# Kernel optimization log

Measured on AMD Instinct MI355X. Metric: run time of the kernel, lower is better.

The kernel has to match this reference:

```python
import jax, jax.numpy as jnp
import numpy as np

N_NODES = 10000
AVG_DEG = 32
N_FEAT = 512
HIDDEN = 32
CODE = 16


def setup_inputs() -> dict:
    key = jax.random.key(0)
    k1, k2, k3, k4, k5 = jax.random.split(key, 5)
    E = N_NODES * AVG_DEG
    src = jax.random.randint(k1, (E,), 0, N_NODES, dtype=jnp.int32)
    dst = jax.random.randint(k2, (E,), 0, N_NODES, dtype=jnp.int32)
    # A + I: add self loops (Kipf & Welling transform)
    loop = jnp.arange(N_NODES, dtype=jnp.int32)
    src = jnp.concatenate([src, loop])
    dst = jnp.concatenate([dst, loop])
    ones = jnp.ones(src.shape[0], jnp.float32)
    deg_row = jax.ops.segment_sum(ones, dst, num_segments=N_NODES)
    deg_col = jax.ops.segment_sum(ones, src, num_segments=N_NODES)
    # symmetric normalization D^-1/2 (A+I) D^-1/2
    edge_weight = jax.lax.rsqrt(deg_row[dst] * deg_col[src])
    x = jax.random.normal(k3, (N_NODES, N_FEAT), dtype=jnp.float32)
    W1 = jax.random.normal(k4, (N_FEAT, HIDDEN), dtype=jnp.float32) * 0.1
    W2 = jax.random.normal(k5, (HIDDEN, CODE), dtype=jnp.float32) * 0.1
    return {"x": x, "W1": W1, "W2": W2, "edge_weight": edge_weight,
            "src": src, "dst": dst}


def _spmm(edge_weight, src, dst, X):
    # sparse A_hat @ X via gather + weighted scatter-add
    return jax.ops.segment_sum(edge_weight[:, None] * X[src], dst,
                               num_segments=X.shape[0])


def reference(x, W1, W2, edge_weight, src, dst):
    # layer 1: A_hat @ (x @ W1), relu  (dropout inactive: eval mode)
    h = jax.nn.relu(_spmm(edge_weight, src, dst, x @ W1))
    # layer 2 (encoder): A_hat @ (h @ W2)
    z = _spmm(edge_weight, src, dst, h @ W2)  # [N, code]
    # inner-product decoder: sigmoid(Z Z^T)
    return jax.nn.sigmoid(jnp.einsum('nc,mc->nm', z, z))
```

## Files before the change

kernel.cpp:

```cpp
#include <hip/hip_runtime.h>
#include <hip/hip_bf16.h>

#define N_NODES 10000
#define N_FEAT  512
#define HIDDEN  32
#define CODE    16

typedef __attribute__((ext_vector_type(8))) short  short8;
typedef __attribute__((ext_vector_type(4))) float  floatx4;

__device__ __forceinline__ float bf2f(unsigned short h) {
    return __uint_as_float(((unsigned int)h) << 16);
}
__device__ __forceinline__ unsigned short f2bf(float f) {
    unsigned int u = __float_as_uint(f);
    u += 0x7fffu + ((u >> 16) & 1u);
    return (unsigned short)(u >> 16);
}
__device__ __forceinline__ float load_f(const void* p, size_t i, int isf32) {
    return isf32 ? ((const float*)p)[i] : bf2f(((const unsigned short*)p)[i]);
}
__device__ __forceinline__ int get_idx(const int* p, int e, int is64) {
    return is64 ? p[2 * (size_t)e] : p[e];
}

__global__ __launch_bounds__(384) void k_detect(const unsigned short* __restrict__ t0,
                                                const unsigned short* __restrict__ t1,
                                                const unsigned short* __restrict__ t2,
                                                const unsigned short* __restrict__ t3,
                                                const int* __restrict__ i0,
                                                const int* __restrict__ i1,
                                                int* __restrict__ flags) {
    const int w    = threadIdx.x >> 6;
    const int lane = threadIdx.x & 63;
    unsigned int m = 0;
    if (w < 4) {
        const unsigned short* p = (w == 0) ? t0 : (w == 1) ? t1 : (w == 2) ? t2 : t3;
        for (int i = lane; i < 128; i += 64) {
            unsigned int v = (unsigned int)p[2 * i] & 0x7fffu;
            m = m > v ? m : v;
        }
    } else {
        const int* p = (w == 4) ? i0 : i1;
        for (int i = lane; i < 128; i += 64) {
            m |= (unsigned int)p[2 * i + 1];
        }
    }
#pragma unroll
    for (int off = 32; off > 0; off >>= 1) {
        unsigned int o = (unsigned int)__shfl_down((int)m, off, 64);
        m = (w < 4) ? (m > o ? m : o) : (m | o);
    }
    if (lane == 0) flags[w] = (w < 4) ? (m >= 0x5000u ? 1 : 0) : (m == 0u ? 1 : 0);
}

__global__ __launch_bounds__(256) void k_xw1(const void* __restrict__ x,
                                             const void* __restrict__ W1,
                                             float* __restrict__ XW1,
                                             const int* __restrict__ flags) {
    const int xf32  = flags[0];
    const int w1f32 = flags[1];
    int t = blockIdx.x * 256 + threadIdx.x;
    if (t >= N_NODES * HIDDEN) return;
    const int n = t >> 5;
    const int c = t & 31;
    float acc = 0.f;
#pragma unroll 8
    for (int k = 0; k < N_FEAT; ++k) {
        float a = load_f(x,  (size_t)n * N_FEAT + k, xf32);
        float b = load_f(W1, (size_t)k * HIDDEN + c, w1f32);
        acc += a * b;
    }
    XW1[t] = acc;
}

__global__ __launch_bounds__(256) void k_spmm32(const void* __restrict__ ew,
                                                const int* __restrict__ src,
                                                const int* __restrict__ dst,
                                                const float* __restrict__ Xin,
                                                float* __restrict__ Hacc, int E,
                                                const int* __restrict__ flags) {
    const int ewf32 = flags[3];
    const int s64   = flags[4];
    const int d64   = flags[5];
    int t = blockIdx.x * 256 + threadIdx.x;
    int e = t >> 5;
    int f = t & 31;
    if (e >= E) return;
    float w = load_f(ew, e, ewf32);
    int   s = get_idx(src, e, s64);
    int   d = get_idx(dst, e, d64);
    float v = Xin[(size_t)s * HIDDEN + f] * w;
    atomicAdd(&Hacc[(size_t)d * HIDDEN + f], v);
}

__global__ __launch_bounds__(256) void k_hw2(const float* __restrict__ H,
                                             const void* __restrict__ W2,
                                             float* __restrict__ HW2,
                                             const int* __restrict__ flags) {
    const int w2f32 = flags[2];
    int t = blockIdx.x * 256 + threadIdx.x;
    if (t >= N_NODES * CODE) return;
    int n = t >> 4;
    int c = t & 15;
    float acc = 0.f;
#pragma unroll
    for (int k = 0; k < HIDDEN; ++k) {
        float h = H[n * HIDDEN + k];
        h = h > 0.f ? h : 0.f;
        acc += h * load_f(W2, k * CODE + c, w2f32);
    }
    HW2[t] = acc;
}

__global__ __launch_bounds__(256) void k_spmm16(const void* __restrict__ ew,
                                                const int* __restrict__ src,
                                                const int* __restrict__ dst,
                                                const float* __restrict__ Hin,
                                                float* __restrict__ Zacc, int E,
                                                const int* __restrict__ flags) {
    const int ewf32 = flags[3];
    const int s64   = flags[4];
    const int d64   = flags[5];
    int t = blockIdx.x * 256 + threadIdx.x;
    int e = t >> 4;
    int f = t & 15;
    if (e >= E) return;
    float w = load_f(ew, e, ewf32);
    int   s = get_idx(src, e, s64);
    int   d = get_idx(dst, e, d64);
    float v = Hin[(size_t)s * CODE + f] * w;
    atomicAdd(&Zacc[(size_t)d * CODE + f], v);
}

__global__ __launch_bounds__(256) void k_cvt(const float* __restrict__ Z,
                                             unsigned short* __restrict__ zb) {
    int t = blockIdx.x * 256 + threadIdx.x;
    if (t >= N_NODES * CODE) return;
    zb[t] = f2bf(Z[t]);
}

__global__ __launch_bounds__(256) void k_dec(const unsigned short* __restrict__ zb,
                                             float* __restrict__ out) {
    const int wave = threadIdx.x >> 6;
    const int lane = threadIdx.x & 63;
    const int l16  = lane & 15;
    const int quad = lane >> 4;

    const int r0 = blockIdx.y * 64 + wave * 16;
    const int c0 = blockIdx.x * 64;

    const short8 zero8 = {0, 0, 0, 0, 0, 0, 0, 0};

    int ra = r0 + l16;
    if (ra > N_NODES - 1) ra = N_NODES - 1;
    short8 afr = zero8;
    if (quad < 2) afr = *(const short8*)(zb + (size_t)ra * CODE + quad * 8);

    floatx4 acc[4];
#pragma unroll
    for (int t = 0; t < 4; ++t) {
        int cb = c0 + t * 16 + l16;
        if (cb > N_NODES - 1) cb = N_NODES - 1;
        short8 bfr = zero8;
        if (quad < 2) bfr = *(const short8*)(zb + (size_t)cb * CODE + quad * 8);
        floatx4 z4 = {0.f, 0.f, 0.f, 0.f};
        acc[t] = __builtin_amdgcn_mfma_f32_16x16x32_bf16(afr, bfr, z4, 0, 0, 0);
    }

#pragma unroll
    for (int t = 0; t < 4; ++t) {
        int col = c0 + t * 16 + l16;
#pragma unroll
        for (int r = 0; r < 4; ++r) {
            int row = r0 + quad * 4 + r;
            float s  = acc[t][r];
            float e  = __builtin_amdgcn_exp2f(-1.442695041f * s);
            float sg = __builtin_amdgcn_rcpf(1.f + e);
            if (row < N_NODES && col < N_NODES) {
                out[(size_t)row * N_NODES + col] = sg;
            }
        }
    }
}

extern "C" void kernel_launch(void* const* d_in, const int* in_sizes, int n_in,
                              void* d_out, int out_size, void* d_ws, size_t ws_size,
                              hipStream_t stream) {
    const void* x  = d_in[0];
    const void* W1 = d_in[1];
    const void* W2 = d_in[2];
    const void* ew = d_in[3];
    const int* src = (const int*)d_in[4];
    const int* dst = (const int*)d_in[5];
    float* out = (float*)d_out;
    const int E = in_sizes[3];

    float* ws   = (float*)d_ws;
    float* XW1  = ws;
    float* Hacc = ws + 320000;
    float* HW2  = ws;
    float* Zacc = ws + 160000;
    unsigned short* zb = (unsigned short*)(ws + 320000);
    int* flags = (int*)(ws + 640000);

    hipMemsetAsync(Hacc, 0, 320000 * sizeof(float), stream);

    k_detect<<<1, 384, 0, stream>>>((const unsigned short*)x,
                                    (const unsigned short*)W1,
                                    (const unsigned short*)W2,
                                    (const unsigned short*)ew,
                                    src, dst, flags);

    k_xw1<<<(N_NODES * HIDDEN + 255) / 256, 256, 0, stream>>>(x, W1, XW1, flags);
    k_spmm32<<<(E * 32 + 255) / 256, 256, 0, stream>>>(ew, src, dst, XW1, Hacc, E, flags);
    hipMemsetAsync(Zacc, 0, 160000 * sizeof(float), stream);
    k_hw2<<<(N_NODES * CODE + 255) / 256, 256, 0, stream>>>(Hacc, W2, HW2, flags);
    k_spmm16<<<(E * 16 + 255) / 256, 256, 0, stream>>>(ew, src, dst, HW2, Zacc, E, flags);
    k_cvt<<<(N_NODES * CODE + 255) / 256, 256, 0, stream>>>(Zacc, zb);

    dim3 grid((N_NODES + 63) / 64, (N_NODES + 63) / 64);
    k_dec<<<grid, 256, 0, stream>>>(zb, out);
}
```

Measured before the change: 569.2 us.

## Replace atomic scatter SpMM with per-call CSR build and row gather

Builds a CSR view of the edges on every call: a histogram of destinations, a single-block scan, and an atomic scatter of source indices and weights. Both SpMM layers then become row-wise gathers with no float atomics. The ReLU is folded into the first gather and the bf16 conversion into the second, which drops a kernel and two memsets. The decoder relies on Z Z^T being symmetric and writes the transposed tile as 4-wide vector stores. The trade-off is three extra small kernels (one of them a serial single-block scan) and a non-deterministic edge order within each row.

```diff
diff --git a/kernel.cpp b/kernel.cpp
--- a/kernel.cpp
+++ b/kernel.cpp
@@ -54,6 +54,60 @@
     if (lane == 0) flags[w] = (w < 4) ? (m >= 0x5000u ? 1 : 0) : (m == 0u ? 1 : 0);
 }
 
+__global__ __launch_bounds__(256) void k_hist(const int* __restrict__ dst,
+                                              int* __restrict__ cnt, int E,
+                                              const int* __restrict__ flags) {
+    const int d64 = flags[5];
+    int t = blockIdx.x * 256 + threadIdx.x;
+    if (t >= E) return;
+    atomicAdd(&cnt[get_idx(dst, t, d64)], 1);
+}
+
+__global__ __launch_bounds__(256) void k_scan(const int* __restrict__ cnt,
+                                              int* __restrict__ rowptr) {
+    __shared__ int sdata[256];
+    const int t = threadIdx.x;
+    const int base = t * 40;
+    int p = 0;
+    for (int j = 0; j < 40; ++j) {
+        int i = base + j;
+        if (i < N_NODES) p += cnt[i];
+    }
+    sdata[t] = p;
+    __syncthreads();
+    for (int off = 1; off < 256; off <<= 1) {
+        int v = (t >= off) ? sdata[t - off] : 0;
+        __syncthreads();
+        sdata[t] += v;
+        __syncthreads();
+    }
+    int run = sdata[t] - p;
+    for (int j = 0; j < 40; ++j) {
+        int i = base + j;
+        if (i < N_NODES) { rowptr[i] = run; run += cnt[i]; }
+    }
+    if (t == 255) rowptr[N_NODES] = sdata[255];
+}
+
+__global__ __launch_bounds__(256) void k_scatter(const int* __restrict__ src,
+                                                 const int* __restrict__ dst,
+                                                 const void* __restrict__ ew,
+                                                 const int* __restrict__ rowptr,
+                                                 int* __restrict__ fill,
+                                                 int* __restrict__ srcS,
+                                                 float* __restrict__ wS, int E,
+                                                 const int* __restrict__ flags) {
+    const int ewf32 = flags[3];
+    const int s64   = flags[4];
+    const int d64   = flags[5];
+    int t = blockIdx.x * 256 + threadIdx.x;
+    if (t >= E) return;
+    int d = get_idx(dst, t, d64);
+    int pos = rowptr[d] + atomicAdd(&fill[d], 1);
+    srcS[pos] = get_idx(src, t, s64);
+    wS[pos]   = load_f(ew, t, ewf32);
+}
+
 __global__ __launch_bounds__(256) void k_xw1(const void* __restrict__ x,
                                              const void* __restrict__ W1,
                                              float* __restrict__ XW1,
@@ -74,24 +128,22 @@
     XW1[t] = acc;
 }
 
-__global__ __launch_bounds__(256) void k_spmm32(const void* __restrict__ ew,
-                                                const int* __restrict__ src,
-                                                const int* __restrict__ dst,
-                                                const float* __restrict__ Xin,
-                                                float* __restrict__ Hacc, int E,
-                                                const int* __restrict__ flags) {
-    const int ewf32 = flags[3];
-    const int s64   = flags[4];
-    const int d64   = flags[5];
-    int t = blockIdx.x * 256 + threadIdx.x;
-    int e = t >> 5;
-    int f = t & 31;
-    if (e >= E) return;
-    float w = load_f(ew, e, ewf32);
-    int   s = get_idx(src, e, s64);
-    int   d = get_idx(dst, e, d64);
-    float v = Xin[(size_t)s * HIDDEN + f] * w;
-    atomicAdd(&Hacc[(size_t)d * HIDDEN + f], v);
+__global__ __launch_bounds__(256) void k_gather32(const int* __restrict__ rowptr,
+                                                  const int* __restrict__ srcS,
+                                                  const float* __restrict__ wS,
+                                                  const float* __restrict__ XW1,
+                                                  float* __restrict__ Hacc) {
+    const int lane = threadIdx.x & 63;
+    const int gw   = blockIdx.x * 4 + (threadIdx.x >> 6);
+    const int n    = gw * 2 + (lane >> 5);
+    const int f    = lane & 31;
+    if (n >= N_NODES) return;
+    const int s0 = rowptr[n], s1 = rowptr[n + 1];
+    float acc = 0.f;
+    for (int j = s0; j < s1; ++j) {
+        acc += wS[j] * XW1[(size_t)srcS[j] * HIDDEN + f];
+    }
+    Hacc[(size_t)n * HIDDEN + f] = fmaxf(acc, 0.f);
 }
 
 __global__ __launch_bounds__(256) void k_hw2(const float* __restrict__ H,
@@ -106,38 +158,27 @@
     float acc = 0.f;
 #pragma unroll
     for (int k = 0; k < HIDDEN; ++k) {
-        float h = H[n * HIDDEN + k];
-        h = h > 0.f ? h : 0.f;
-        acc += h * load_f(W2, k * CODE + c, w2f32);
+        acc += H[n * HIDDEN + k] * load_f(W2, k * CODE + c, w2f32);
     }
     HW2[t] = acc;
 }
 
-__global__ __launch_bounds__(256) void k_spmm16(const void* __restrict__ ew,
-                                                const int* __restrict__ src,
-                                                const int* __restrict__ dst,
-                                                const float* __restrict__ Hin,
-                                                float* __restrict__ Zacc, int E,
-                                                const int* __restrict__ flags) {
-    const int ewf32 = flags[3];
-    const int s64   = flags[4];
-    const int d64   = flags[5];
-    int t = blockIdx.x * 256 + threadIdx.x;
-    int e = t >> 4;
-    int f = t & 15;
-    if (e >= E) return;
-    float w = load_f(ew, e, ewf32);
-    int   s = get_idx(src, e, s64);
-    int   d = get_idx(dst, e, d64);
-    float v = Hin[(size_t)s * CODE + f] * w;
-    atomicAdd(&Zacc[(size_t)d * CODE + f], v);
-}
-
-__global__ __launch_bounds__(256) void k_cvt(const float* __restrict__ Z,
-                                             unsigned short* __restrict__ zb) {
-    int t = blockIdx.x * 256 + threadIdx.x;
-    if (t >= N_NODES * CODE) return;
-    zb[t] = f2bf(Z[t]);
+__global__ __launch_bounds__(256) void k_gather16(const int* __restrict__ rowptr,
+                                                  const int* __restrict__ srcS,
+                                                  const float* __restrict__ wS,
+                                                  const float* __restrict__ HW2,
+                                                  unsigned short* __restrict__ zb) {
+    const int lane = threadIdx.x & 63;
+    const int gw   = blockIdx.x * 4 + (threadIdx.x >> 6);
+    const int n    = gw * 4 + (lane >> 4);
+    const int f    = lane & 15;
+    if (n >= N_NODES) return;
+    const int s0 = rowptr[n], s1 = rowptr[n + 1];
+    float acc = 0.f;
+    for (int j = s0; j < s1; ++j) {
+        acc += wS[j] * HW2[(size_t)srcS[j] * CODE + f];
+    }
+    zb[(size_t)n * CODE + f] = f2bf(acc);
 }
 
 __global__ __launch_bounds__(256) void k_dec(const unsigned short* __restrict__ zb,
@@ -168,18 +209,19 @@
         acc[t] = __builtin_amdgcn_mfma_f32_16x16x32_bf16(afr, bfr, z4, 0, 0, 0);
     }
 
+    const int rb = r0 + quad * 4;
 #pragma unroll
     for (int t = 0; t < 4; ++t) {
         int col = c0 + t * 16 + l16;
+        floatx4 v;
 #pragma unroll
         for (int r = 0; r < 4; ++r) {
-            int row = r0 + quad * 4 + r;
-            float s  = acc[t][r];
-            float e  = __builtin_amdgcn_exp2f(-1.442695041f * s);
-            float sg = __builtin_amdgcn_rcpf(1.f + e);
-            if (row < N_NODES && col < N_NODES) {
-                out[(size_t)row * N_NODES + col] = sg;
-            }
+            float s = acc[t][r];
+            float e = __builtin_amdgcn_exp2f(-1.442695041f * s);
+            v[r] = __builtin_amdgcn_rcpf(1.f + e);
+        }
+        if (col < N_NODES && rb < N_NODES) {
+            *(floatx4*)(out + (size_t)col * N_NODES + rb) = v;
         }
     }
 }
@@ -200,11 +242,15 @@
     float* XW1  = ws;
     float* Hacc = ws + 320000;
     float* HW2  = ws;
-    float* Zacc = ws + 160000;
     unsigned short* zb = (unsigned short*)(ws + 320000);
-    int* flags = (int*)(ws + 640000);
-
-    hipMemsetAsync(Hacc, 0, 320000 * sizeof(float), stream);
+    int* flags  = (int*)(ws + 640000);
+    int* cnt    = (int*)(ws + 700000);
+    int* fill   = (int*)(ws + 710000);
+    int* rowptr = (int*)(ws + 720000);
+    int* srcS   = (int*)(ws + 730016);
+    float* wS   = (float*)(srcS + E);
+
+    hipMemsetAsync(cnt, 0, 20000 * sizeof(int), stream);
 
     k_detect<<<1, 384, 0, stream>>>((const unsigned short*)x,
                                     (const unsigned short*)W1,
@@ -212,12 +258,15 @@
                                     (const unsigned short*)ew,
                                     src, dst, flags);
 
-    k_xw1<<<(N_NODES * HIDDEN + 255) / 256, 256, 0, stream>>>(x, W1, XW1, flags);
-    k_spmm32<<<(E * 32 + 255) / 256, 256, 0, stream>>>(ew, src, dst, XW1, Hacc, E, flags);
-    hipMemsetAsync(Zacc, 0, 160000 * sizeof(float), stream);
-    k_hw2<<<(N_NODES * CODE + 255) / 256, 256, 0, stream>>>(Hacc, W2, HW2, flags);
-    k_spmm16<<<(E * 16 + 255) / 256, 256, 0, stream>>>(ew, src, dst, HW2, Zacc, E, flags);
-    k_cvt<<<(N_NODES * CODE + 255) / 256, 256, 0, stream>>>(Zacc, zb);
+    k_hist   <<<(E + 255) / 256, 256, 0, stream>>>(dst, cnt, E, flags);
+    k_scan   <<<1, 256, 0, stream>>>(cnt, rowptr);
+    k_scatter<<<(E + 255) / 256, 256, 0, stream>>>(src, dst, ew, rowptr, fill,
+                                                   srcS, wS, E, flags);
+
+    k_xw1     <<<(N_NODES * HIDDEN + 255) / 256, 256, 0, stream>>>(x, W1, XW1, flags);
+    k_gather32<<<(N_NODES + 7) / 8, 256, 0, stream>>>(rowptr, srcS, wS, XW1, Hacc);
+    k_hw2     <<<(N_NODES * CODE + 255) / 256, 256, 0, stream>>>(Hacc, W2, HW2, flags);
+    k_gather16<<<(N_NODES + 15) / 16, 256, 0, stream>>>(rowptr, srcS, wS, HW2, zb);
 
     dim3 grid((N_NODES + 63) / 64, (N_NODES + 63) / 64);
     k_dec<<<grid, 256, 0, stream>>>(zb, out);
```

Measured after the change: 572.0 us. No clear change (+0.5%).
